# Performance work log

Measured on AMD Instinct MI355X. Metric: run time of the kernel, lower is better.

The kernel has to match this reference:

```python
import jax, jax.numpy as jnp
import numpy as np

B, N, D, H = 2, 2048, 1024, 16
DK = D // H


def setup_inputs() -> dict:
    key = jax.random.key(0)
    ks = jax.random.split(key, 8)
    s = 1.0 / np.sqrt(D)  # keep projection outputs O(1)
    return {
        "x": jax.random.normal(ks[0], (B, N, D), jnp.float32),
        "alpha": jax.random.uniform(ks[1], (B, N), jnp.float32, -1.0, 1.0),
        "bias": jax.random.normal(ks[2], (B, N, N), jnp.float32) * 0.1,
        "Wq": jax.random.normal(ks[3], (D, D), jnp.float32) * s,
        "bq": jnp.zeros((D,), jnp.float32),
        "Wk": jax.random.normal(ks[4], (D, D), jnp.float32) * s,
        "bk": jnp.zeros((D,), jnp.float32),
        "Wv": jax.random.normal(ks[5], (D, D), jnp.float32) * s,
        "bv": jnp.zeros((D,), jnp.float32),
        "Wo": jax.random.normal(ks[6], (D, D), jnp.float32) * s,
        "bo": jnp.zeros((D,), jnp.float32),
    }


def reference(x, alpha, bias, Wq, bq, Wk, bk, Wv, bv, Wo, bo):
    b, n, d = x.shape
    # projections -> (B, H, N, DK)
    def split_heads(t):
        return t.reshape(b, n, H, DK).transpose(0, 2, 1, 3)

    q = split_heads(x @ Wq + bq)
    k = split_heads(x @ Wk + bk)
    v = split_heads(x @ Wv + bv)

    # salience rescale of keys/values: (B,1,N,1)
    scale = 1.0 + alpha[:, None, :, None]
    k = k * scale
    v = v * scale

    logits = jnp.einsum("bhnd,bhmd->bhnm", q, k) / np.float32(np.sqrt(DK))
    logits = logits + bias[:, None, :, :]  # broadcast over heads
    attn = jax.nn.softmax(logits, axis=-1)

    y = jnp.einsum("bhnm,bhmd->bhnd", attn, v)
    y = y.transpose(0, 2, 1, 3).reshape(b, n, d)
    return y @ Wo + bo
```

## Files before the change

kernel.cpp:

```cpp
#include <hip/hip_runtime.h>

typedef __attribute__((ext_vector_type(8))) short bf16x8;
typedef __attribute__((ext_vector_type(4))) float f32x4;

#define LOG2E 1.4426950408889634f

static __device__ __forceinline__ unsigned short f2bf(float f) {
    unsigned int u = __builtin_bit_cast(unsigned int, f);
    u += 0x7fffu + ((u >> 16) & 1u);
    return (unsigned short)(u >> 16);
}
static __device__ __forceinline__ float bf2f(unsigned short h) {
    unsigned int u = ((unsigned int)h) << 16;
    return __builtin_bit_cast(float, u);
}
static __device__ __forceinline__ void gload_lds16(const void* g, void* l) {
    __builtin_amdgcn_global_load_lds(
        (const __attribute__((address_space(1))) void*)g,
        (__attribute__((address_space(3))) void*)l, 16, 0, 0);
}

__global__ void convert_bf16(const float* __restrict__ src,
                             unsigned short* __restrict__ dst, int n8) {
    int i = blockIdx.x * blockDim.x + threadIdx.x;
    if (i >= n8) return;
    const float4* s4 = (const float4*)src;
    float4 a = s4[2 * i], b = s4[2 * i + 1];
    uint4 u;
    u.x = (unsigned)f2bf(a.x) | ((unsigned)f2bf(a.y) << 16);
    u.y = (unsigned)f2bf(a.z) | ((unsigned)f2bf(a.w) << 16);
    u.z = (unsigned)f2bf(b.x) | ((unsigned)f2bf(b.y) << 16);
    u.w = (unsigned)f2bf(b.z) | ((unsigned)f2bf(b.w) << 16);
    *(uint4*)(dst + 8 * (size_t)i) = u;
}

__global__ void bias_permute(const float* __restrict__ src,
                             unsigned short* __restrict__ dst) {
    int mt = blockIdx.x, qt = blockIdx.y, b = blockIdx.z;
    int tid = threadIdx.x, w = tid >> 6, lane = tid & 63;
    int quad = lane >> 4, l16 = lane & 15;
    const float* s = src + (size_t)b * 2048 * 2048;
    unsigned short* d = dst + (((size_t)(b * 16 + qt) * 32 + mt) * 8192);
    for (int e = 0; e < 2; e++) {
        unsigned short vals[16];
        for (int c = 0; c < 4; c++)
            for (int r = 0; r < 4; r++) {
                int q = qt * 128 + e * 64 + w * 16 + quad * 4 + r;
                int k = mt * 64 + c * 16 + l16;
                vals[c * 4 + r] = f2bf(s[(size_t)q * 2048 + k] * LOG2E);
            }
        unsigned short* o = d + ((size_t)((e * 4 + w) * 64 + lane)) * 16;
        *(bf16x8*)&o[0] = *(bf16x8*)&vals[0];
        *(bf16x8*)&o[8] = *(bf16x8*)&vals[8];
    }
}

__global__ void transpose_convert4(const float* __restrict__ W0,
                                   const float* __restrict__ W1,
                                   const float* __restrict__ W2,
                                   const float* __restrict__ W3,
                                   unsigned short* __restrict__ T0,
                                   unsigned short* __restrict__ T1,
                                   unsigned short* __restrict__ T2,
                                   unsigned short* __restrict__ T3) {
    const float* W = (blockIdx.z == 0) ? W0 : (blockIdx.z == 1) ? W1
                     : (blockIdx.z == 2) ? W2 : W3;
    unsigned short* Wt = (blockIdx.z == 0) ? T0 : (blockIdx.z == 1) ? T1
                         : (blockIdx.z == 2) ? T2 : T3;
    __shared__ float t[32][33];
    int tx = threadIdx.x, ty = threadIdx.y;
    int x0 = blockIdx.x * 32, y0 = blockIdx.y * 32;
    for (int i = 0; i < 4; i++)
        t[ty + 8 * i][tx] = W[(size_t)(y0 + ty + 8 * i) * 1024 + x0 + tx];
    __syncthreads();
    for (int i = 0; i < 4; i++)
        Wt[(size_t)(x0 + ty + 8 * i) * 1024 + y0 + tx] = f2bf(t[tx][ty + 8 * i]);
}

__launch_bounds__(256)
__global__ void gemm_qkv(const unsigned short* __restrict__ A,
                         const unsigned short* __restrict__ WqT,
                         const unsigned short* __restrict__ WkT,
                         const unsigned short* __restrict__ WvT,
                         const float* __restrict__ bq,
                         const float* __restrict__ bk,
                         const float* __restrict__ bv,
                         const float* __restrict__ alpha,
                         unsigned short* __restrict__ Qb,
                         unsigned short* __restrict__ Kb,
                         unsigned short* __restrict__ Vtb) {
    int which = blockIdx.y >> 3;
    const unsigned short* Bt = (which == 0) ? WqT : (which == 1) ? WkT : WvT;
    const float* bias = (which == 0) ? bq : (which == 1) ? bk : bv;

    __shared__ __align__(16) unsigned short As[128][64];
    __shared__ __align__(16) unsigned short Bs[128][64];
    int tid = threadIdx.x;
    int wave = tid >> 6, lane = tid & 63, quad = lane >> 4, l16 = lane & 15;
    int wm = wave & 1, wn = wave >> 1;
    int lrow = lane >> 3, lblk = lane & 7;
    int swz = ((lblk ^ lrow) * 8);
    int m0 = blockIdx.x * 128, n0 = (blockIdx.y & 7) * 128;
    f32x4 acc[4][4] = {};

    for (int kt = 0; kt < 16; kt++) {
        int k0 = kt * 64;
        for (int i = 0; i < 4; i++) {
            int rbase = i * 32 + wave * 8;
            gload_lds16(&A[(size_t)(m0 + rbase + lrow) * 1024 + k0 + swz],
                        &As[rbase][0]);
            gload_lds16(&Bt[(size_t)(n0 + rbase + lrow) * 1024 + k0 + swz],
                        &Bs[rbase][0]);
        }
        __syncthreads();
        for (int ks = 0; ks < 2; ks++) {
            int pblk = ((ks * 4 + quad) ^ (l16 & 7)) * 8;
            bf16x8 af[4], bf_[4];
            for (int i = 0; i < 4; i++)
                af[i] = *(const bf16x8*)&As[64 * wm + 16 * i + l16][pblk];
            for (int j = 0; j < 4; j++)
                bf_[j] = *(const bf16x8*)&Bs[64 * wn + 16 * j + l16][pblk];
            if (which == 2) {
                for (int i = 0; i < 4; i++)
                    for (int j = 0; j < 4; j++)
                        acc[i][j] = __builtin_amdgcn_mfma_f32_16x16x32_bf16(
                            af[i], bf_[j], acc[i][j], 0, 0, 0);
            } else {
                for (int i = 0; i < 4; i++)
                    for (int j = 0; j < 4; j++)
                        acc[i][j] = __builtin_amdgcn_mfma_f32_16x16x32_bf16(
                            bf_[j], af[i], acc[i][j], 0, 0, 0);
            }
        }
        __syncthreads();
    }

    if (which == 2) {
        for (int i = 0; i < 4; i++)
            for (int j = 0; j < 4; j++) {
                int colb = n0 + 64 * wn + 16 * j + l16;
                int h = colb >> 6, dk = colb & 63;
                int row0 = m0 + 64 * wm + 16 * i + quad * 4;
                int bb = row0 >> 11, nn0 = row0 & 2047;
                unsigned short v4[4];
                for (int r = 0; r < 4; r++) {
                    float v = acc[i][j][r] + bias[colb];
                    v4[r] = f2bf(v * (1.0f + alpha[bb * 2048 + nn0 + r]));
                }
                uint2 u;
                u.x = (unsigned)v4[0] | ((unsigned)v4[1] << 16);
                u.y = (unsigned)v4[2] | ((unsigned)v4[3] << 16);
                *(uint2*)&Vtb[((size_t)(bb * 16 + h) * 64 + dk) * 2048 + nn0] = u;
            }
    } else {
        unsigned short* outb = (which == 0) ? Qb : Kb;
        for (int i = 0; i < 4; i++)
            for (int j = 0; j < 4; j++) {
                int row = m0 + 64 * wm + 16 * i + l16;
                int bb = row >> 11, nn = row & 2047;
                int colb0 = n0 + 64 * wn + 16 * j + quad * 4;
                int h = colb0 >> 6, dk0 = colb0 & 63;
                float4 b4 = *(const float4*)&bias[colb0];
                float s = (which == 0) ? (0.125f * LOG2E)
                                       : (1.0f + alpha[bb * 2048 + nn]);
                unsigned short v4[4];
                v4[0] = f2bf((acc[i][j][0] + b4.x) * s);
                v4[1] = f2bf((acc[i][j][1] + b4.y) * s);
                v4[2] = f2bf((acc[i][j][2] + b4.z) * s);
                v4[3] = f2bf((acc[i][j][3] + b4.w) * s);
                uint2 u;
                u.x = (unsigned)v4[0] | ((unsigned)v4[1] << 16);
                u.y = (unsigned)v4[2] | ((unsigned)v4[3] << 16);
                *(uint2*)&outb[((size_t)(bb * 16 + h) * 2048 + nn) * 64 + dk0] = u;
            }
    }
}

__launch_bounds__(256)
__global__ void gemm_out(const unsigned short* __restrict__ A,
                         const unsigned short* __restrict__ Bt,
                         const float* __restrict__ bias,
                         float* __restrict__ outf) {
    __shared__ __align__(16) unsigned short As[128][64];
    __shared__ __align__(16) unsigned short Bs[128][64];
    int tid = threadIdx.x;
    int wave = tid >> 6, lane = tid & 63, quad = lane >> 4, l16 = lane & 15;
    int wm = wave & 1, wn = wave >> 1;
    int lrow = lane >> 3, lblk = lane & 7;
    int swz = ((lblk ^ lrow) * 8);
    int m0 = blockIdx.x * 128, n0 = blockIdx.y * 128;
    f32x4 acc[4][4] = {};

    for (int kt = 0; kt < 16; kt++) {
        int k0 = kt * 64;
        for (int i = 0; i < 4; i++) {
            int rbase = i * 32 + wave * 8;
            gload_lds16(&A[(size_t)(m0 + rbase + lrow) * 1024 + k0 + swz],
                        &As[rbase][0]);
            gload_lds16(&Bt[(size_t)(n0 + rbase + lrow) * 1024 + k0 + swz],
                        &Bs[rbase][0]);
        }
        __syncthreads();
        for (int ks = 0; ks < 2; ks++) {
            int pblk = ((ks * 4 + quad) ^ (l16 & 7)) * 8;
            bf16x8 af[4], bf_[4];
            for (int i = 0; i < 4; i++)
                af[i] = *(const bf16x8*)&As[64 * wm + 16 * i + l16][pblk];
            for (int j = 0; j < 4; j++)
                bf_[j] = *(const bf16x8*)&Bs[64 * wn + 16 * j + l16][pblk];
            for (int i = 0; i < 4; i++)
                for (int j = 0; j < 4; j++)
                    acc[i][j] = __builtin_amdgcn_mfma_f32_16x16x32_bf16(
                        bf_[j], af[i], acc[i][j], 0, 0, 0);
        }
        __syncthreads();
    }

    for (int i = 0; i < 4; i++)
        for (int j = 0; j < 4; j++) {
            int row = m0 + 64 * wm + 16 * i + l16;
            int colb0 = n0 + 64 * wn + 16 * j + quad * 4;
            float4 b4 = *(const float4*)&bias[colb0];
            float4 o;
            o.x = acc[i][j][0] + b4.x;
            o.y = acc[i][j][1] + b4.y;
            o.z = acc[i][j][2] + b4.z;
            o.w = acc[i][j][3] + b4.w;
            *(float4*)&outf[(size_t)row * 1024 + colb0] = o;
        }
}

__launch_bounds__(256, 4)
__global__ void attn_kernel(const unsigned short* __restrict__ Q,
                            const unsigned short* __restrict__ K,
                            const unsigned short* __restrict__ Vt,
                            const unsigned short* __restrict__ biasP,
                            unsigned short* __restrict__ Y,
                            float* __restrict__ Opart,
                            float* __restrict__ Lpart, int split) {
    __shared__ __align__(16) unsigned short Ks[64][64];
    __shared__ __align__(16) unsigned short Vs[64][64];
    __shared__ __align__(16) unsigned short Ps[4][32][72];
    int tid = threadIdx.x;
    int wave = tid >> 6, lane = tid & 63, quad = lane >> 4, l16 = lane & 15;
    int qt = blockIdx.x, h = blockIdx.y;
    int b, mt0, mtN;
    if (split) { b = blockIdx.z >> 1; int half = blockIdx.z & 1;
                 mt0 = half * 16; mtN = mt0 + 16; }
    else       { b = blockIdx.z; mt0 = 0; mtN = 32; }
    int q0 = qt * 128;
    size_t headoff = (size_t)(b * 16 + h) * 2048 * 64;
    const unsigned short* Kp = K + headoff;
    const unsigned short* Vp = Vt + headoff;
    int lrow = lane >> 3, lblk = lane & 7;
    int swz = (lblk ^ lrow) * 8;

    bf16x8 aq[2][2];
    for (int e = 0; e < 2; e++) {
        const unsigned short* qp =
            Q + headoff + (size_t)(q0 + e * 64 + wave * 16 + l16) * 64;
        aq[e][0] = *(const bf16x8*)&qp[quad * 8];
        aq[e][1] = *(const bf16x8*)&qp[32 + quad * 8];
    }
    bf16x8 ones;
    for (int j = 0; j < 8; j++) ones[j] = (short)0x3F80;

    f32x4 oacc[2][4] = {};
    f32x4 lacc[2] = {};
    const unsigned short* bP = biasP + (size_t)(b * 16 + qt) * 32 * 8192;

    for (int mt = mt0; mt < mtN; mt++) {
        int m0 = mt * 64;
        for (int i = 0; i < 2; i++) {
            int rbase = wave * 16 + i * 8;
            gload_lds16(&Kp[(size_t)(m0 + rbase + lrow) * 64 + swz], &Ks[rbase][0]);
            gload_lds16(&Vp[(size_t)(rbase + lrow) * 2048 + m0 + swz], &Vs[rbase][0]);
        }
        const unsigned short* bt = bP + (size_t)mt * 8192;
        bf16x8 bz[2][2];
        for (int e = 0; e < 2; e++) {
            const unsigned short* p = bt + (size_t)((e * 4 + wave) * 64 + lane) * 16;
            bz[e][0] = *(const bf16x8*)&p[0];
            bz[e][1] = *(const bf16x8*)&p[8];
        }
        __syncthreads();

        f32x4 sc[2][4];
        for (int e = 0; e < 2; e++)
            for (int c = 0; c < 4; c++) {
                f32x4 s;
                for (int r = 0; r < 4; r++)
                    s[r] = bf2f(((unsigned short*)&bz[e][c >> 1])[(c & 1) * 4 + r]);
                sc[e][c] = s;
            }
        for (int c = 0; c < 4; c++) {
            for (int ks = 0; ks < 2; ks++) {
                bf16x8 kf = *(const bf16x8*)&Ks[c * 16 + l16]
                                               [((ks * 4 + quad) ^ (l16 & 7)) * 8];
                sc[0][c] = __builtin_amdgcn_mfma_f32_16x16x32_bf16(aq[0][ks], kf, sc[0][c], 0, 0, 0);
                sc[1][c] = __builtin_amdgcn_mfma_f32_16x16x32_bf16(aq[1][ks], kf, sc[1][c], 0, 0, 0);
            }
        }

        for (int e = 0; e < 2; e++)
            for (int c = 0; c < 4; c++) {
                int colw = (((c * 2 + (l16 >> 3)) + quad) & 7) * 8 + (l16 & 7);
                for (int r = 0; r < 4; r++) {
                    float p = exp2f(sc[e][c][r]);
                    unsigned int u = __builtin_bit_cast(unsigned int, p);
                    Ps[wave][e * 16 + quad * 4 + r][colw] = (unsigned short)(u >> 16);
                }
            }

        for (int ks = 0; ks < 2; ks++) {
            int blkr = (ks * 4 + quad + (l16 >> 2)) & 7;
            bf16x8 pf0 = *(const bf16x8*)&Ps[wave][l16][blkr * 8];
            bf16x8 pf1 = *(const bf16x8*)&Ps[wave][16 + l16][blkr * 8];
            lacc[0] = __builtin_amdgcn_mfma_f32_16x16x32_bf16(pf0, ones, lacc[0], 0, 0, 0);
            lacc[1] = __builtin_amdgcn_mfma_f32_16x16x32_bf16(pf1, ones, lacc[1], 0, 0, 0);
            for (int cv = 0; cv < 4; cv++) {
                bf16x8 vf = *(const bf16x8*)&Vs[cv * 16 + l16]
                                               [((ks * 4 + quad) ^ (l16 & 7)) * 8];
                oacc[0][cv] = __builtin_amdgcn_mfma_f32_16x16x32_bf16(pf0, vf, oacc[0][cv], 0, 0, 0);
                oacc[1][cv] = __builtin_amdgcn_mfma_f32_16x16x32_bf16(pf1, vf, oacc[1][cv], 0, 0, 0);
            }
        }
        __syncthreads();
    }

    if (split) {
        size_t p = ((size_t)((b * 16 + h) * 16 + qt)) * 2 + (blockIdx.z & 1);
        float* Op = Opart + p * 8192;
        for (int e = 0; e < 2; e++)
            for (int cv = 0; cv < 4; cv++)
                for (int r = 0; r < 4; r++)
                    Op[(e * 64 + wave * 16 + quad * 4 + r) * 64 + cv * 16 + l16] =
                        oacc[e][cv][r];
        if (l16 == 0)
            for (int e = 0; e < 2; e++)
                for (int r = 0; r < 4; r++)
                    Lpart[p * 128 + e * 64 + wave * 16 + quad * 4 + r] = lacc[e][r];
    } else {
        for (int e = 0; e < 2; e++) {
            float invl[4];
            for (int r = 0; r < 4; r++) invl[r] = 1.0f / lacc[e][r];
            for (int cv = 0; cv < 4; cv++)
                for (int r = 0; r < 4; r++) {
                    int qrow = q0 + e * 64 + 16 * wave + quad * 4 + r;
                    int d = h * 64 + cv * 16 + l16;
                    Y[((size_t)b * 2048 + qrow) * 1024 + d] =
                        f2bf(oacc[e][cv][r] * invl[r]);
                }
        }
    }
}

__global__ void attn_combine(const float* __restrict__ Opart,
                             const float* __restrict__ Lpart,
                             unsigned short* __restrict__ Y) {
    int blk = blockIdx.x;
    int qt = blk & 15, h = (blk >> 4) & 15, b = blk >> 8;
    const float* O0 = Opart + (size_t)blk * 2 * 8192;
    const float* O1 = O0 + 8192;
    const float* L0 = Lpart + (size_t)blk * 2 * 128;
    const float* L1 = L0 + 128;
    int t = threadIdx.x;
    for (int i = 0; i < 8; i++) {
        int idx4 = i * 256 + t;
        int q = idx4 >> 4;
        int dk = (idx4 & 15) * 4;
        float4 a = *(const float4*)&O0[idx4 * 4];
        float4 c = *(const float4*)&O1[idx4 * 4];
        float inv = 1.0f / (L0[q] + L1[q]);
        uint2 u;
        u.x = (unsigned)f2bf((a.x + c.x) * inv) |
              ((unsigned)f2bf((a.y + c.y) * inv) << 16);
        u.y = (unsigned)f2bf((a.z + c.z) * inv) |
              ((unsigned)f2bf((a.w + c.w) * inv) << 16);
        int qrow = qt * 128 + q;
        *(uint2*)&Y[((size_t)b * 2048 + qrow) * 1024 + h * 64 + dk] = u;
    }
}

extern "C" void kernel_launch(void* const* d_in, const int* in_sizes, int n_in,
                              void* d_out, int out_size, void* d_ws, size_t ws_size,
                              hipStream_t stream) {
    const float* x     = (const float*)d_in[0];
    const float* alpha = (const float*)d_in[1];
    const float* bias  = (const float*)d_in[2];
    const float* Wq    = (const float*)d_in[3];
    const float* bq    = (const float*)d_in[4];
    const float* Wk    = (const float*)d_in[5];
    const float* bk    = (const float*)d_in[6];
    const float* Wv    = (const float*)d_in[7];
    const float* bv    = (const float*)d_in[8];
    const float* Wo    = (const float*)d_in[9];
    const float* bo    = (const float*)d_in[10];
    float* out = (float*)d_out;

    char* ws = (char*)d_ws;
    const size_t MB = 1048576;
    unsigned short* xb    = (unsigned short*)(ws);
    unsigned short* wqt   = (unsigned short*)(ws + 8 * MB);
    unsigned short* wkt   = (unsigned short*)(ws + 10 * MB);
    unsigned short* wvt   = (unsigned short*)(ws + 12 * MB);
    unsigned short* wot   = (unsigned short*)(ws + 14 * MB);
    unsigned short* Qb    = (unsigned short*)(ws + 16 * MB);
    unsigned short* Kb    = (unsigned short*)(ws + 24 * MB);
    unsigned short* Vtb   = (unsigned short*)(ws + 32 * MB);
    unsigned short* biasP = (unsigned short*)(ws + 40 * MB);
    float*          Opart = (float*)(ws + 56 * MB);
    float*          Lpart = (float*)(ws + 88 * MB);
    unsigned short* Yb    = xb;
    int split = (ws_size >= 90 * MB) ? 1 : 0;

    convert_bf16<<<2048, 256, 0, stream>>>(x, xb, 524288);
    bias_permute<<<dim3(32, 16, 2), 256, 0, stream>>>(bias, biasP);
    transpose_convert4<<<dim3(32, 32, 4), dim3(32, 8), 0, stream>>>(
        Wq, Wk, Wv, Wo, wqt, wkt, wvt, wot);

    gemm_qkv<<<dim3(32, 24), 256, 0, stream>>>(
        xb, wqt, wkt, wvt, bq, bk, bv, alpha, Qb, Kb, Vtb);

    if (split) {
        attn_kernel<<<dim3(16, 16, 4), 256, 0, stream>>>(
            Qb, Kb, Vtb, biasP, Yb, Opart, Lpart, 1);
        attn_combine<<<512, 256, 0, stream>>>(Opart, Lpart, Yb);
    } else {
        attn_kernel<<<dim3(16, 16, 2), 256, 0, stream>>>(
            Qb, Kb, Vtb, biasP, Yb, Opart, Lpart, 0);
    }

    gemm_out<<<dim3(32, 8), 256, 0, stream>>>(Yb, wot, bo, out);
}
```

Measured before the change: 251.3 us.

## Transpose score MFMA layout to vectorize P stores and bias loads

```diff
diff --git a/kernel.cpp b/kernel.cpp
--- a/kernel.cpp
+++ b/kernel.cpp
@@ -42,13 +42,16 @@
     const float* s = src + (size_t)b * 2048 * 2048;
     unsigned short* d = dst + (((size_t)(b * 16 + qt) * 32 + mt) * 8192);
     for (int e = 0; e < 2; e++) {
+        int q = qt * 128 + e * 64 + w * 16 + l16;
         unsigned short vals[16];
-        for (int c = 0; c < 4; c++)
-            for (int r = 0; r < 4; r++) {
-                int q = qt * 128 + e * 64 + w * 16 + quad * 4 + r;
-                int k = mt * 64 + c * 16 + l16;
-                vals[c * 4 + r] = f2bf(s[(size_t)q * 2048 + k] * LOG2E);
-            }
+        for (int c = 0; c < 4; c++) {
+            const float* p = &s[(size_t)q * 2048 + mt * 64 + c * 16 + quad * 4];
+            float4 v = *(const float4*)p;
+            vals[c * 4 + 0] = f2bf(v.x * LOG2E);
+            vals[c * 4 + 1] = f2bf(v.y * LOG2E);
+            vals[c * 4 + 2] = f2bf(v.z * LOG2E);
+            vals[c * 4 + 3] = f2bf(v.w * LOG2E);
+        }
         unsigned short* o = d + ((size_t)((e * 4 + w) * 64 + lane)) * 16;
         *(bf16x8*)&o[0] = *(bf16x8*)&vals[0];
         *(bf16x8*)&o[8] = *(bf16x8*)&vals[8];
@@ -297,25 +300,28 @@
             for (int ks = 0; ks < 2; ks++) {
                 bf16x8 kf = *(const bf16x8*)&Ks[c * 16 + l16]
                                                [((ks * 4 + quad) ^ (l16 & 7)) * 8];
-                sc[0][c] = __builtin_amdgcn_mfma_f32_16x16x32_bf16(aq[0][ks], kf, sc[0][c], 0, 0, 0);
-                sc[1][c] = __builtin_amdgcn_mfma_f32_16x16x32_bf16(aq[1][ks], kf, sc[1][c], 0, 0, 0);
-            }
-        }
-
-        for (int e = 0; e < 2; e++)
+                sc[0][c] = __builtin_amdgcn_mfma_f32_16x16x32_bf16(kf, aq[0][ks], sc[0][c], 0, 0, 0);
+                sc[1][c] = __builtin_amdgcn_mfma_f32_16x16x32_bf16(kf, aq[1][ks], sc[1][c], 0, 0, 0);
+            }
+        }
+
+        for (int e = 0; e < 2; e++) {
+            unsigned short* prow = &Ps[wave][e * 16 + l16][quad * 4];
             for (int c = 0; c < 4; c++) {
-                int colw = (((c * 2 + (l16 >> 3)) + quad) & 7) * 8 + (l16 & 7);
-                for (int r = 0; r < 4; r++) {
-                    float p = exp2f(sc[e][c][r]);
-                    unsigned int u = __builtin_bit_cast(unsigned int, p);
-                    Ps[wave][e * 16 + quad * 4 + r][colw] = (unsigned short)(u >> 16);
-                }
-            }
+                unsigned int b0 = __builtin_bit_cast(unsigned int, exp2f(sc[e][c][0]));
+                unsigned int b1 = __builtin_bit_cast(unsigned int, exp2f(sc[e][c][1]));
+                unsigned int b2 = __builtin_bit_cast(unsigned int, exp2f(sc[e][c][2]));
+                unsigned int b3 = __builtin_bit_cast(unsigned int, exp2f(sc[e][c][3]));
+                uint2 u;
+                u.x = (b0 >> 16) | (b1 & 0xffff0000u);
+                u.y = (b2 >> 16) | (b3 & 0xffff0000u);
+                *(uint2*)&prow[c * 16] = u;
+            }
+        }
 
         for (int ks = 0; ks < 2; ks++) {
-            int blkr = (ks * 4 + quad + (l16 >> 2)) & 7;
-            bf16x8 pf0 = *(const bf16x8*)&Ps[wave][l16][blkr * 8];
-            bf16x8 pf1 = *(const bf16x8*)&Ps[wave][16 + l16][blkr * 8];
+            bf16x8 pf0 = *(const bf16x8*)&Ps[wave][l16][ks * 32 + quad * 8];
+            bf16x8 pf1 = *(const bf16x8*)&Ps[wave][16 + l16][ks * 32 + quad * 8];
             lacc[0] = __builtin_amdgcn_mfma_f32_16x16x32_bf16(pf0, ones, lacc[0], 0, 0, 0);
             lacc[1] = __builtin_amdgcn_mfma_f32_16x16x32_bf16(pf1, ones, lacc[1], 0, 0, 0);
             for (int cv = 0; cv < 4; cv++) {
```

After: 248.3 us. Within noise of the previous version (-1.2%).

## Double-buffer K/V tiles and prefetch bias in attention loop

Applied to the files above, without the earlier changes.

```diff
diff --git a/kernel.cpp b/kernel.cpp
--- a/kernel.cpp
+++ b/kernel.cpp
@@ -230,7 +230,7 @@
         }
 }
 
-__launch_bounds__(256, 4)
+__launch_bounds__(256, 3)
 __global__ void attn_kernel(const unsigned short* __restrict__ Q,
                             const unsigned short* __restrict__ K,
                             const unsigned short* __restrict__ Vt,
@@ -238,8 +238,8 @@
                             unsigned short* __restrict__ Y,
                             float* __restrict__ Opart,
                             float* __restrict__ Lpart, int split) {
-    __shared__ __align__(16) unsigned short Ks[64][64];
-    __shared__ __align__(16) unsigned short Vs[64][64];
+    __shared__ __align__(16) unsigned short Ks[2][64][64];
+    __shared__ __align__(16) unsigned short Vs[2][64][64];
     __shared__ __align__(16) unsigned short Ps[4][32][72];
     int tid = threadIdx.x;
     int wave = tid >> 6, lane = tid & 63, quad = lane >> 4, l16 = lane & 15;
@@ -269,33 +269,63 @@
     f32x4 lacc[2] = {};
     const unsigned short* bP = biasP + (size_t)(b * 16 + qt) * 32 * 8192;
 
-    for (int mt = mt0; mt < mtN; mt++) {
-        int m0 = mt * 64;
+    {
+        int m0 = mt0 * 64;
         for (int i = 0; i < 2; i++) {
             int rbase = wave * 16 + i * 8;
-            gload_lds16(&Kp[(size_t)(m0 + rbase + lrow) * 64 + swz], &Ks[rbase][0]);
-            gload_lds16(&Vp[(size_t)(rbase + lrow) * 2048 + m0 + swz], &Vs[rbase][0]);
-        }
-        const unsigned short* bt = bP + (size_t)mt * 8192;
-        bf16x8 bz[2][2];
+            gload_lds16(&Kp[(size_t)(m0 + rbase + lrow) * 64 + swz],
+                        &Ks[0][rbase][0]);
+            gload_lds16(&Vp[(size_t)(rbase + lrow) * 2048 + m0 + swz],
+                        &Vs[0][rbase][0]);
+        }
+    }
+    bf16x8 bz[2][2];
+    {
+        const unsigned short* bt = bP + (size_t)mt0 * 8192;
         for (int e = 0; e < 2; e++) {
             const unsigned short* p = bt + (size_t)((e * 4 + wave) * 64 + lane) * 16;
             bz[e][0] = *(const bf16x8*)&p[0];
             bz[e][1] = *(const bf16x8*)&p[8];
         }
-        __syncthreads();
+    }
+    __syncthreads();
+
+    for (int mt = mt0; mt < mtN; mt++) {
+        int cur = (mt - mt0) & 1;
+
+        bf16x8 bzn[2][2];
+        if (mt + 1 < mtN) {
+            int m1 = (mt + 1) * 64;
+            for (int i = 0; i < 2; i++) {
+                int rbase = wave * 16 + i * 8;
+                gload_lds16(&Kp[(size_t)(m1 + rbase + lrow) * 64 + swz],
+                            &Ks[cur ^ 1][rbase][0]);
+                gload_lds16(&Vp[(size_t)(rbase + lrow) * 2048 + m1 + swz],
+                            &Vs[cur ^ 1][rbase][0]);
+            }
+            const unsigned short* bt = bP + (size_t)(mt + 1) * 8192;
+            for (int e = 0; e < 2; e++) {
+                const unsigned short* p =
+                    bt + (size_t)((e * 4 + wave) * 64 + lane) * 16;
+                bzn[e][0] = *(const bf16x8*)&p[0];
+                bzn[e][1] = *(const bf16x8*)&p[8];
+            }
+        }
 
         f32x4 sc[2][4];
         for (int e = 0; e < 2; e++)
             for (int c = 0; c < 4; c++) {
+                uint2 w = ((const uint2*)&bz[e][c >> 1])[c & 1];
                 f32x4 s;
-                for (int r = 0; r < 4; r++)
-                    s[r] = bf2f(((unsigned short*)&bz[e][c >> 1])[(c & 1) * 4 + r]);
+                s[0] = __builtin_bit_cast(float, w.x << 16);
+                s[1] = __builtin_bit_cast(float, w.x & 0xffff0000u);
+                s[2] = __builtin_bit_cast(float, w.y << 16);
+                s[3] = __builtin_bit_cast(float, w.y & 0xffff0000u);
                 sc[e][c] = s;
             }
         for (int c = 0; c < 4; c++) {
             for (int ks = 0; ks < 2; ks++) {
-                bf16x8 kf = *(const bf16x8*)&Ks[c * 16 + l16]
+                bf16x8 kf = *(const bf16x8*)&Ks[cur][c * 16 + l16]
                                                [((ks * 4 + quad) ^ (l16 & 7)) * 8];
                 sc[0][c] = __builtin_amdgcn_mfma_f32_16x16x32_bf16(aq[0][ks], kf, sc[0][c], 0, 0, 0);
                 sc[1][c] = __builtin_amdgcn_mfma_f32_16x16x32_bf16(aq[1][ks], kf, sc[1][c], 0, 0, 0);
@@ -319,11 +349,16 @@
             lacc[0] = __builtin_amdgcn_mfma_f32_16x16x32_bf16(pf0, ones, lacc[0], 0, 0, 0);
             lacc[1] = __builtin_amdgcn_mfma_f32_16x16x32_bf16(pf1, ones, lacc[1], 0, 0, 0);
             for (int cv = 0; cv < 4; cv++) {
-                bf16x8 vf = *(const bf16x8*)&Vs[cv * 16 + l16]
+                bf16x8 vf = *(const bf16x8*)&Vs[cur][cv * 16 + l16]
                                                [((ks * 4 + quad) ^ (l16 & 7)) * 8];
                 oacc[0][cv] = __builtin_amdgcn_mfma_f32_16x16x32_bf16(pf0, vf, oacc[0][cv], 0, 0, 0);
                 oacc[1][cv] = __builtin_amdgcn_mfma_f32_16x16x32_bf16(pf1, vf, oacc[1][cv], 0, 0, 0);
             }
+        }
+
+        if (mt + 1 < mtN) {
+            bz[0][0] = bzn[0][0]; bz[0][1] = bzn[0][1];
+            bz[1][0] = bzn[1][0]; bz[1][1] = bzn[1][1];
         }
         __syncthreads();
     }
```

After: 258.4 us. 2.8% more time.
